# Kernel tuning notes

Hardware: AMD Instinct MI355X
Metric: run time of the kernel (lower is better)

## Reference

```python
import jax, jax.numpy as jnp
import numpy as np

B, D_IN, H1, H2, A = 8192, 512, 4096, 4096, 64
QMIN, QMAX = -128.0, 127.0  # int8 saturation range


def _int_vals(key, shape, spread):
    # integer-valued fixed-point tensor stored as float32
    return jnp.clip(jnp.round(jax.random.normal(key, shape) * spread), QMIN * spread, QMAX * spread).astype(jnp.float32)


def setup_inputs() -> dict:
    key = jax.random.key(0)
    ks = jax.random.split(key, 9)
    x = jnp.clip(jnp.round(jax.random.normal(ks[0], (B, D_IN)) * 32.0), QMIN, QMAX).astype(jnp.float32)
    w1 = jnp.clip(jnp.round(jax.random.normal(ks[1], (H1, D_IN)) * 16.0), QMIN, QMAX).astype(jnp.float32)
    b1 = _int_vals(ks[2], (H1,), 256.0)
    w2 = jnp.clip(jnp.round(jax.random.normal(ks[3], (H2, H1)) * 16.0), QMIN, QMAX).astype(jnp.float32)
    b2 = _int_vals(ks[4], (H2,), 256.0)
    w_mu = jnp.clip(jnp.round(jax.random.normal(ks[5], (A, H2)) * 16.0), QMIN, QMAX).astype(jnp.float32)
    b_mu = _int_vals(ks[6], (A,), 256.0)
    w_prob = jnp.clip(jnp.round(jax.random.normal(ks[7], (A, H2)) * 16.0), QMIN, QMAX).astype(jnp.float32)
    b_prob = _int_vals(ks[8], (A,), 256.0)
    M = jnp.full((1,), 2.0 ** -10, dtype=jnp.float32)  # per-layer requant multiplier
    s = jnp.full((1,), 0.05, dtype=jnp.float32)        # activation quantize scale
    return {
        "x": x, "w1": w1, "b1": b1, "w2": w2, "b2": b2,
        "w_mu": w_mu, "b_mu": b_mu, "w_prob": w_prob, "b_prob": b_prob,
        "M1": M, "M2": M, "M_mu": M, "M_prob": M,
        "s2": s, "s_mu": s, "s_prob": s,
    }


def _qlinear(x, w, b, M):
    # genesys fixed-point linear: int accumulate then requantize by multiplier M
    acc = jnp.matmul(x, w.T) + b  # integer-valued fp32 accumulator
    return jnp.round(M * acc)


def _quantize(src, scale, zero_point=0.0):
    return jnp.clip(jnp.round(src / scale) + zero_point, QMIN, QMAX)


def reference(x, w1, b1, w2, b2, w_mu, b_mu, w_prob, b_prob, M1, M2, M_mu, M_prob, s2, s_mu, s_prob):
    h = jax.nn.relu(_qlinear(x, w1, b1, M1))
    h = _quantize(h, s2)
    h = jax.nn.relu(_qlinear(h, w2, b2, M2))
    # NOTE: original forward_int feeds the un-quantized relu output into the
    # heads (x_mu/x_prob quantizations are dead code) and returns only prob.
    prob = _qlinear(h, w_prob, b_prob, M_prob)
    return prob
```

## Files before the change

kernel.cpp:

```cpp
#include <hip/hip_runtime.h>
#include <stdint.h>

#define NB   8192
#define DIN  512
#define NH1  4096
#define NH2  4096
#define NA   64

typedef int v4i __attribute__((ext_vector_type(4)));

__device__ __forceinline__ v4i mfma_i8(v4i a, v4i b, v4i c) {
    return __builtin_amdgcn_mfma_i32_16x16x64_i8(a, b, c, 0, 0, 0);
}

__device__ __forceinline__ void gload16(const void* g, const void* l) {
    __builtin_amdgcn_global_load_lds(
        (const __attribute__((address_space(1))) void*)(uintptr_t)g,
        (__attribute__((address_space(3))) void*)(uint32_t)(uintptr_t)l,
        16, 0, 0);
}

__global__ void cvt_i8(const float* __restrict__ in, signed char* __restrict__ out, int n4) {
    const int i = blockIdx.x * blockDim.x + threadIdx.x;
    if (i >= n4) return;
    const float4 v = ((const float4*)in)[i];
    char4 c;
    c.x = (signed char)__float2int_rn(v.x);
    c.y = (signed char)__float2int_rn(v.y);
    c.z = (signed char)__float2int_rn(v.z);
    c.w = (signed char)__float2int_rn(v.w);
    ((char4*)out)[i] = c;
}

__global__ void cvt_xfrag(const float* __restrict__ x, signed char* __restrict__ xf) {
    const int u   = blockIdx.x * 256 + threadIdx.x;
    const int g   = u >> 9;
    const int rem = u & 511;
    const int kt  = rem >> 6;
    const int l   = rem & 63;
    const int row = g * 16 + (l & 15);
    const int k0  = kt * 64 + (l >> 4) * 16;
    const float4* src = (const float4*)(x + (size_t)row * DIN + k0);
    signed char v[16];
    #pragma unroll
    for (int q = 0; q < 4; ++q) {
        const float4 f = src[q];
        v[q*4+0] = (signed char)__float2int_rn(f.x);
        v[q*4+1] = (signed char)__float2int_rn(f.y);
        v[q*4+2] = (signed char)__float2int_rn(f.z);
        v[q*4+3] = (signed char)__float2int_rn(f.w);
    }
    *(int4*)(xf + (size_t)u * 16) = *(const int4*)v;
}

__global__ void sum_wp(const float* __restrict__ wp, int* __restrict__ S) {
    __shared__ int red[256];
    const int a = blockIdx.x, t = threadIdx.x;
    int p = 0;
    for (int k = t; k < NH2; k += 256) p += __float2int_rn(wp[(size_t)a * NH2 + k]);
    red[t] = p; __syncthreads();
    for (int s = 128; s > 0; s >>= 1) { if (t < s) red[t] += red[t + s]; __syncthreads(); }
    if (t == 0) S[a] = red[0];
}

template <int EPI>
__global__ __launch_bounds__(512, 4)
void gemm_af(const signed char* __restrict__ Af,
             const signed char* __restrict__ Bg,
             int M, int N, int K,
             const float* __restrict__ bias,
             const float* __restrict__ Mscale,
             const float* __restrict__ qscale,
             signed char* __restrict__ out0,
             signed char* __restrict__ out1)
{
    __shared__ __align__(16) signed char lds[69632];

    const int tid  = threadIdx.x;
    const int lane = tid & 63;
    const int wid  = tid >> 6;
    const int wm   = wid >> 1, wn = wid & 1;

    const int nwg  = gridDim.x;
    const int bid  = blockIdx.x;
    const int swzb = (bid & 7) * (nwg >> 3) + (bid >> 3);
    const int nbx  = N >> 7;
    const int bx   = swzb % nbx;
    const int by   = swzb / nbx;
    const int bm0  = by << 8, bn0 = bx << 7;

    const int srow = tid >> 2;
    const int sc   = (((tid & 3) ^ ((tid >> 3) & 3)) << 4);
    const signed char* bS = Bg + (size_t)(bn0 + srow) * K + sc;

    const int r    = lane & 15;
    const int pc   = (((lane >> 4) ^ ((r >> 1) & 3)) << 4);
    const int boff = wn * 4096 + r * 64 + pc;

    const int NKT = K >> 6;
    const signed char* afB = Af + (((size_t)((bm0 >> 4) + wm * 4) * NKT) << 10) + lane * 16;

    const int nt = K >> 6;

    v4i af[4], bf[4];
    #pragma unroll
    for (int m = 0; m < 4; ++m)
        af[m] = *(const v4i*)(afB + (((size_t)(m * NKT)) << 10));
    gload16(bS,      lds + tid * 16);
    gload16(bS + 64, lds + 8192 + tid * 16);
    asm volatile("s_waitcnt vmcnt(1)" ::: "memory");
    __builtin_amdgcn_s_barrier();

    v4i acc[4][4] = {};

    for (int t = 0; t < nt; ++t) {
        const signed char* L = lds + (t % 3) * 8192;
        #pragma unroll
        for (int n = 0; n < 4; ++n) bf[n] = *(const v4i*)(L + boff + n * 1024);

        const size_t tl = (size_t)((t + 1 < nt) ? (t + 1) : t);

        __builtin_amdgcn_s_setprio(1);
        #pragma unroll
        for (int m = 0; m < 4; ++m) {
            #pragma unroll
            for (int n = 0; n < 4; ++n)
                acc[m][n] = mfma_i8(af[m], bf[n], acc[m][n]);
            af[m] = *(const v4i*)(afB + (((size_t)(m * NKT) + tl) << 10));
        }
        __builtin_amdgcn_s_setprio(0);

        if (t + 2 < nt) {
            gload16(bS + ((t + 2) << 6), lds + ((t + 2) % 3) * 8192 + tid * 16);
            asm volatile("s_waitcnt vmcnt(1)" ::: "memory");
        } else if (t + 1 < nt) {
            asm volatile("s_waitcnt vmcnt(0)" ::: "memory");
        }
        __builtin_amdgcn_s_barrier();
    }

    __syncthreads();
    signed char* img0 = lds;
    signed char* img1 = lds + 34816;
    const int rowb = wm * 64 + ((lane >> 4) << 2);
    const int colb = wn * 64 + (lane & 15);

    if constexpr (EPI == 1) {
        const float Mv = Mscale[0];
        const float sv = qscale[0];
        #pragma unroll
        for (int n = 0; n < 4; ++n) {
            const int col  = colb + n * 16;
            const int bint = __float2int_rn(bias[bn0 + col]);
            #pragma unroll
            for (int m = 0; m < 4; ++m) {
                #pragma unroll
                for (int j = 0; j < 4; ++j) {
                    const int row  = rowb + m * 16 + j;
                    const int accv = acc[m][n][j] + bint;
                    float h = rintf(Mv * (float)accv);
                    h = fmaxf(h, 0.0f);
                    float q = rintf(h / sv);
                    q = fminf(fmaxf(q, -128.0f), 127.0f);
                    img0[row * 136 + col] = (signed char)(int)q;
                }
            }
        }
        __syncthreads();
        const int oNKT = N >> 6;
        #pragma unroll
        for (int i = 0; i < 4; ++i) {
            const int u    = i * 512 + tid;
            const int g_l  = u >> 7;
            const int kt_l = (u >> 6) & 1;
            const int l    = u & 63;
            const int lrow = g_l * 16 + (l & 15);
            const int lcol = kt_l * 64 + (l >> 4) * 16;
            const size_t g  = (size_t)((bm0 >> 4) + g_l);
            const size_t kt = (size_t)((bn0 >> 6) + kt_l);
            *(int4*)(out0 + ((g * oNKT + kt) << 10) + l * 16) =
                *(const int4*)(img0 + lrow * 136 + lcol);
        }
    } else {
        const float Mv = Mscale[0];
        #pragma unroll
        for (int n = 0; n < 4; ++n) {
            const int col  = colb + n * 16;
            const int bint = __float2int_rn(bias[bn0 + col]);
            #pragma unroll
            for (int m = 0; m < 4; ++m) {
                #pragma unroll
                for (int j = 0; j < 4; ++j) {
                    const int row  = rowb + m * 16 + j;
                    const int accv = acc[m][n][j] + bint;
                    double rr = rint((double)Mv * (double)accv);
                    rr = rr > 0.0 ? rr : 0.0;
                    const int v = (int)rr;
                    img0[row * 136 + col] = (signed char)((v & 255) - 128);
                    img1[row * 136 + col] = (signed char)((v >> 8) - 128);
                }
            }
        }
        __syncthreads();
        #pragma unroll
        for (int p = 0; p < 8; ++p) {
            const int idx = p * 512 + tid;
            const int row = idx >> 4;
            const int cb  = (idx & 15) * 8;
            const size_t gaddr = (size_t)(bm0 + row) * N + bn0 + cb;
            *(int2*)(out0 + gaddr) = *(const int2*)(img0 + row * 136 + cb);
            *(int2*)(out1 + gaddr) = *(const int2*)(img1 + row * 136 + cb);
        }
    }
}

__global__ __launch_bounds__(512, 1)
void head_mfma(const signed char* __restrict__ lo,
               const signed char* __restrict__ hi,
               const signed char* __restrict__ wpq,
               int* __restrict__ part)
{
    __shared__ __align__(16) signed char Bl[32768];
    __shared__ __align__(16) signed char Al[3][32768];

    const int tid  = threadIdx.x;
    const int lane = tid & 63;
    const int wid  = tid >> 6;
    const int rblk = blockIdx.x >> 3;
    const int kblk = blockIdx.x & 7;
    const int bm0  = rblk << 8;
    const int kb   = kblk << 9;

    #pragma unroll
    for (int s = 0; s < 4; ++s) {
        const int brow = s * 16 + (tid >> 5);
        const int pch  = tid & 31;
        const int lc   = pch ^ (brow & 7);
        gload16(wpq + (size_t)brow * NH2 + kb + lc * 16, Bl + brow * 512 + pch * 16);
    }

    const int srow  = tid >> 2;
    const int sclog = (tid & 3) ^ ((tid >> 3) & 3);
    const size_t ab = (size_t)(bm0 + srow) * NH2 + kb + sclog * 16;
    const size_t rK = (size_t)128 * NH2;

    #define HSTAGE(bp, ko) do { \
        gload16(lo + ab + (ko),      &Al[bp][0]     + tid * 16); \
        gload16(lo + ab + rK + (ko), &Al[bp][8192]  + tid * 16); \
        gload16(hi + ab + (ko),      &Al[bp][16384] + tid * 16); \
        gload16(hi + ab + rK + (ko), &Al[bp][24576] + tid * 16); } while (0)

    HSTAGE(0, 0);
    HSTAGE(1, 64);

    const int r    = lane & 15;
    const int cg   = lane >> 4;
    const int pcA  = (cg ^ ((r >> 1) & 3)) * 16;
    const int aoff = wid * 2048 + r * 64 + pcA;

    v4i accL[2][4] = {}, accH[2][4] = {};
    int cur = 0, nxt = 2;

    for (int t = 0; t < 8; ++t) {
        if (t < 7) asm volatile("s_waitcnt vmcnt(4)" ::: "memory");
        else       asm volatile("s_waitcnt vmcnt(0)" ::: "memory");
        __builtin_amdgcn_s_barrier();

        const signed char* A = &Al[cur][0];
        v4i bf[4], al[2], ah[2];
        #pragma unroll
        for (int n = 0; n < 4; ++n)
            bf[n] = *(const v4i*)(Bl + (n * 16 + r) * 512 + (((t * 4 + cg) ^ (r & 7)) * 16));
        #pragma unroll
        for (int m = 0; m < 2; ++m) al[m] = *(const v4i*)(A + aoff + m * 1024);
        #pragma unroll
        for (int m = 0; m < 2; ++m) ah[m] = *(const v4i*)(A + 16384 + aoff + m * 1024);

        if (t + 2 < 8) HSTAGE(nxt, (t + 2) << 6);

        __builtin_amdgcn_s_setprio(1);
        #pragma unroll
        for (int m = 0; m < 2; ++m)
            #pragma unroll
            for (int n = 0; n < 4; ++n) {
                accL[m][n] = mfma_i8(al[m], bf[n], accL[m][n]);
                accH[m][n] = mfma_i8(ah[m], bf[n], accH[m][n]);
            }
        __builtin_amdgcn_s_setprio(0);
        __builtin_amdgcn_s_barrier();

        cur = (cur == 2) ? 0 : cur + 1;
        nxt = (nxt == 2) ? 0 : nxt + 1;
    }
    #undef HSTAGE

    int* pb = part + (size_t)kblk * (NB * NA);
    const int rowb = bm0 + wid * 32 + ((lane >> 4) << 2);
    #pragma unroll
    for (int m = 0; m < 2; ++m)
        #pragma unroll
        for (int n = 0; n < 4; ++n) {
            const int a = n * 16 + (lane & 15);
            #pragma unroll
            for (int j = 0; j < 4; ++j) {
                const int row = rowb + m * 16 + j;
                pb[(size_t)row * NA + a] = accL[m][n][j] + (accH[m][n][j] << 8);
            }
        }
}

__global__ __launch_bounds__(256)
void comb_head(const int* __restrict__ part, const int* __restrict__ S,
               const float* __restrict__ bp, const float* __restrict__ Mp,
               float* __restrict__ out)
{
    const int t = blockIdx.x * 256 + threadIdx.x;
    const int a = t & 63;
    long long sum = 0;
    #pragma unroll
    for (int c = 0; c < 8; ++c) sum += part[(size_t)c * (NB * NA) + t];
    sum += 32896LL * (long long)S[a] + (long long)__float2int_rn(bp[a]);
    out[t] = (float)rint((double)Mp[0] * (double)sum);
}

extern "C" void kernel_launch(void* const* d_in, const int* in_sizes, int n_in,
                              void* d_out, int out_size, void* d_ws, size_t ws_size,
                              hipStream_t stream) {
    const float* x  = (const float*)d_in[0];
    const float* w1 = (const float*)d_in[1];
    const float* b1 = (const float*)d_in[2];
    const float* w2 = (const float*)d_in[3];
    const float* b2 = (const float*)d_in[4];
    const float* wp = (const float*)d_in[7];
    const float* bp = (const float*)d_in[8];
    const float* M1 = (const float*)d_in[9];
    const float* M2 = (const float*)d_in[10];
    const float* Mp = (const float*)d_in[12];
    const float* s2 = (const float*)d_in[13];

    const size_t MB = (size_t)1 << 20;
    char* ws = (char*)d_ws;
    signed char* xf    = (signed char*)(ws);
    signed char* w1_i8 = (signed char*)(ws + 4  * MB);
    signed char* w2_i8 = (signed char*)(ws + 6  * MB);
    signed char* wp_i8 = (signed char*)(ws + 22 * MB);
    int*         Ssum  = (int*)        (ws + 22 * MB + 512 * 1024);
    signed char* h1f   = (signed char*)(ws + 23 * MB);
    signed char* h2lo  = (signed char*)(ws + 55 * MB);
    signed char* h2hi  = (signed char*)(ws + 87 * MB);
    int*         part  = (int*)        (ws);

    cvt_xfrag<<<dim3(1024), dim3(256), 0, stream>>>(x, xf);
    cvt_i8<<<dim3(2048),  dim3(256), 0, stream>>>(w1, w1_i8, NH1 * DIN / 4);
    cvt_i8<<<dim3(16384), dim3(256), 0, stream>>>(w2, w2_i8, NH2 * NH1 / 4);
    cvt_i8<<<dim3(256),   dim3(256), 0, stream>>>(wp, wp_i8, NA  * NH2 / 4);
    sum_wp<<<dim3(64), dim3(256), 0, stream>>>(wp, Ssum);

    gemm_af<1><<<dim3((NB / 256) * (NH1 / 128)), dim3(512), 0, stream>>>(
        xf, w1_i8, NB, NH1, DIN, b1, M1, s2, h1f, nullptr);
    gemm_af<2><<<dim3((NB / 256) * (NH2 / 128)), dim3(512), 0, stream>>>(
        h1f, w2_i8, NB, NH2, NH1, b2, M2, nullptr, h2lo, h2hi);
    head_mfma<<<dim3(256), dim3(512), 0, stream>>>(h2lo, h2hi, wp_i8, part);
    comb_head<<<dim3(NB * NA / 256), dim3(256), 0, stream>>>(part, Ssum, bp, Mp, (float*)d_out);
}
```

Before: 208.8 us.

## Fuse prob head into layer-2 GEMM epilogue with atomic accumulation; merge prep kernels

Removes the separate head_mfma kernel. Each layer-2 GEMM tile now multiplies its lo/hi split int8 activations, held in LDS, by the matching K-slice of the fragment-ordered head weights, then atomically adds 64-bit partial sums into a zeroed buffer. This avoids writing the two 32 MB h2 planes to global memory and reading them back. The four conversion kernels and the weight-sum kernel are merged into one launch, and the LDS row stride changes from 136 to 144. The cost is heavy 64-bit global atomic traffic, since each output element gets one add per N-tile (32 per element), plus an extra memset.

```diff
diff --git a/kernel.cpp b/kernel.cpp
--- a/kernel.cpp
+++ b/kernel.cpp
@@ -20,47 +20,72 @@
         16, 0, 0);
 }
 
-__global__ void cvt_i8(const float* __restrict__ in, signed char* __restrict__ out, int n4) {
-    const int i = blockIdx.x * blockDim.x + threadIdx.x;
-    if (i >= n4) return;
-    const float4 v = ((const float4*)in)[i];
-    char4 c;
-    c.x = (signed char)__float2int_rn(v.x);
-    c.y = (signed char)__float2int_rn(v.y);
-    c.z = (signed char)__float2int_rn(v.z);
-    c.w = (signed char)__float2int_rn(v.w);
-    ((char4*)out)[i] = c;
-}
-
-__global__ void cvt_xfrag(const float* __restrict__ x, signed char* __restrict__ xf) {
-    const int u   = blockIdx.x * 256 + threadIdx.x;
-    const int g   = u >> 9;
-    const int rem = u & 511;
-    const int kt  = rem >> 6;
-    const int l   = rem & 63;
-    const int row = g * 16 + (l & 15);
-    const int k0  = kt * 64 + (l >> 4) * 16;
-    const float4* src = (const float4*)(x + (size_t)row * DIN + k0);
-    signed char v[16];
-    #pragma unroll
-    for (int q = 0; q < 4; ++q) {
-        const float4 f = src[q];
-        v[q*4+0] = (signed char)__float2int_rn(f.x);
-        v[q*4+1] = (signed char)__float2int_rn(f.y);
-        v[q*4+2] = (signed char)__float2int_rn(f.z);
-        v[q*4+3] = (signed char)__float2int_rn(f.w);
+__global__ __launch_bounds__(256)
+void prep(const float* __restrict__ x,  const float* __restrict__ w1,
+          const float* __restrict__ w2, const float* __restrict__ wp,
+          signed char* __restrict__ xf, signed char* __restrict__ w1_i8,
+          signed char* __restrict__ w2_i8, signed char* __restrict__ wpf,
+          int* __restrict__ S)
+{
+    __shared__ int red[256];
+    const int b   = blockIdx.x;
+    const int tid = threadIdx.x;
+
+    if (b < 18432) {
+        const float* in  = (b < 16384) ? w2 : w1;
+        signed char* out = (b < 16384) ? w2_i8 : w1_i8;
+        const int i = ((b < 16384) ? b : (b - 16384)) * 256 + tid;
+        const float4 v = ((const float4*)in)[i];
+        char4 c;
+        c.x = (signed char)__float2int_rn(v.x);
+        c.y = (signed char)__float2int_rn(v.y);
+        c.z = (signed char)__float2int_rn(v.z);
+        c.w = (signed char)__float2int_rn(v.w);
+        ((char4*)out)[i] = c;
+    } else if (b < 19456) {
+        const int u   = (b - 18432) * 256 + tid;
+        const int g   = u >> 9;
+        const int kt  = (u >> 6) & 7;
+        const int l   = u & 63;
+        const int row = g * 16 + (l & 15);
+        const int k0  = kt * 64 + (l >> 4) * 16;
+        const float4* src = (const float4*)(x + (size_t)row * DIN + k0);
+        signed char v[16];
+        #pragma unroll
+        for (int q = 0; q < 4; ++q) {
+            const float4 f = src[q];
+            v[q*4+0] = (signed char)__float2int_rn(f.x);
+            v[q*4+1] = (signed char)__float2int_rn(f.y);
+            v[q*4+2] = (signed char)__float2int_rn(f.z);
+            v[q*4+3] = (signed char)__float2int_rn(f.w);
+        }
+        *(int4*)(xf + (size_t)u * 16) = *(const int4*)v;
+    } else if (b < 19520) {
+        const int u   = (b - 19456) * 256 + tid;
+        const int g   = u >> 12;
+        const int kt  = (u >> 6) & 63;
+        const int l   = u & 63;
+        const int row = g * 16 + (l & 15);
+        const int k0  = kt * 64 + (l >> 4) * 16;
+        const float4* src = (const float4*)(wp + (size_t)row * NH2 + k0);
+        signed char v[16];
+        #pragma unroll
+        for (int q = 0; q < 4; ++q) {
+            const float4 f = src[q];
+            v[q*4+0] = (signed char)__float2int_rn(f.x);
+            v[q*4+1] = (signed char)__float2int_rn(f.y);
+            v[q*4+2] = (signed char)__float2int_rn(f.z);
+            v[q*4+3] = (signed char)__float2int_rn(f.w);
+        }
+        *(int4*)(wpf + (size_t)u * 16) = *(const int4*)v;
+    } else {
+        const int a = b - 19520;
+        int p = 0;
+        for (int k = tid; k < NH2; k += 256) p += __float2int_rn(wp[(size_t)a * NH2 + k]);
+        red[tid] = p; __syncthreads();
+        for (int s = 128; s > 0; s >>= 1) { if (tid < s) red[tid] += red[tid + s]; __syncthreads(); }
+        if (tid == 0) S[a] = red[0];
     }
-    *(int4*)(xf + (size_t)u * 16) = *(const int4*)v;
-}
-
-__global__ void sum_wp(const float* __restrict__ wp, int* __restrict__ S) {
-    __shared__ int red[256];
-    const int a = blockIdx.x, t = threadIdx.x;
-    int p = 0;
-    for (int k = t; k < NH2; k += 256) p += __float2int_rn(wp[(size_t)a * NH2 + k]);
-    red[t] = p; __syncthreads();
-    for (int s = 128; s > 0; s >>= 1) { if (t < s) red[t] += red[t + s]; __syncthreads(); }
-    if (t == 0) S[a] = red[0];
 }
 
 template <int EPI>
@@ -72,9 +97,10 @@
              const float* __restrict__ Mscale,
              const float* __restrict__ qscale,
              signed char* __restrict__ out0,
-             signed char* __restrict__ out1)
+             const signed char* __restrict__ wpf,
+             unsigned long long* __restrict__ part)
 {
-    __shared__ __align__(16) signed char lds[69632];
+    __shared__ __align__(16) signed char lds[73728];
 
     const int tid  = threadIdx.x;
     const int lane = tid & 63;
@@ -141,7 +167,7 @@
 
     __syncthreads();
     signed char* img0 = lds;
-    signed char* img1 = lds + 34816;
+    signed char* img1 = lds + 36864;
     const int rowb = wm * 64 + ((lane >> 4) << 2);
     const int colb = wn * 64 + (lane & 15);
 
@@ -162,7 +188,7 @@
                     h = fmaxf(h, 0.0f);
                     float q = rintf(h / sv);
                     q = fminf(fmaxf(q, -128.0f), 127.0f);
-                    img0[row * 136 + col] = (signed char)(int)q;
+                    img0[row * 144 + col] = (signed char)(int)q;
                 }
             }
         }
@@ -179,7 +205,7 @@
             const size_t g  = (size_t)((bm0 >> 4) + g_l);
             const size_t kt = (size_t)((bn0 >> 6) + kt_l);
             *(int4*)(out0 + ((g * oNKT + kt) << 10) + l * 16) =
-                *(const int4*)(img0 + lrow * 136 + lcol);
+                *(const int4*)(img0 + lrow * 144 + lcol);
         }
     } else {
         const float Mv = Mscale[0];
@@ -196,129 +222,60 @@
                     double rr = rint((double)Mv * (double)accv);
                     rr = rr > 0.0 ? rr : 0.0;
                     const int v = (int)rr;
-                    img0[row * 136 + col] = (signed char)((v & 255) - 128);
-                    img1[row * 136 + col] = (signed char)((v >> 8) - 128);
+                    img0[row * 144 + col] = (signed char)((v & 255) - 128);
+                    img1[row * 144 + col] = (signed char)((v >> 8) - 128);
                 }
             }
         }
         __syncthreads();
-        #pragma unroll
-        for (int p = 0; p < 8; ++p) {
-            const int idx = p * 512 + tid;
-            const int row = idx >> 4;
-            const int cb  = (idx & 15) * 8;
-            const size_t gaddr = (size_t)(bm0 + row) * N + bn0 + cb;
-            *(int2*)(out0 + gaddr) = *(const int2*)(img0 + row * 136 + cb);
-            *(int2*)(out1 + gaddr) = *(const int2*)(img1 + row * 136 + cb);
+
+        v4i bh[4][2];
+        #pragma unroll
+        for (int n = 0; n < 4; ++n)
+            #pragma unroll
+            for (int kk = 0; kk < 2; ++kk)
+                bh[n][kk] = *(const v4i*)(wpf + (((size_t)(n * 64 + (bn0 >> 6) + kk)) << 10) + lane * 16);
+
+        v4i accL[2][4] = {}, accH[2][4] = {};
+        #pragma unroll
+        for (int mm = 0; mm < 2; ++mm) {
+            const int arow = (wid * 2 + mm) * 16 + (lane & 15);
+            #pragma unroll
+            for (int kk = 0; kk < 2; ++kk) {
+                const int ka = kk * 64 + (lane >> 4) * 16;
+                const v4i aL = *(const v4i*)(img0 + arow * 144 + ka);
+                const v4i aH = *(const v4i*)(img1 + arow * 144 + ka);
+                #pragma unroll
+                for (int n = 0; n < 4; ++n) {
+                    accL[mm][n] = mfma_i8(aL, bh[n][kk], accL[mm][n]);
+                    accH[mm][n] = mfma_i8(aH, bh[n][kk], accH[mm][n]);
+                }
+            }
+        }
+        #pragma unroll
+        for (int mm = 0; mm < 2; ++mm) {
+            #pragma unroll
+            for (int n = 0; n < 4; ++n) {
+                const int a = n * 16 + (lane & 15);
+                #pragma unroll
+                for (int j = 0; j < 4; ++j) {
+                    const int row = bm0 + (wid * 2 + mm) * 16 + ((lane >> 4) << 2) + j;
+                    const long long val = (long long)accL[mm][n][j] + 256LL * (long long)accH[mm][n][j];
+                    atomicAdd(part + (size_t)row * NA + a, (unsigned long long)val);
+                }
+            }
         }
     }
 }
 
-__global__ __launch_bounds__(512, 1)
-void head_mfma(const signed char* __restrict__ lo,
-               const signed char* __restrict__ hi,
-               const signed char* __restrict__ wpq,
-               int* __restrict__ part)
-{
-    __shared__ __align__(16) signed char Bl[32768];
-    __shared__ __align__(16) signed char Al[3][32768];
-
-    const int tid  = threadIdx.x;
-    const int lane = tid & 63;
-    const int wid  = tid >> 6;
-    const int rblk = blockIdx.x >> 3;
-    const int kblk = blockIdx.x & 7;
-    const int bm0  = rblk << 8;
-    const int kb   = kblk << 9;
-
-    #pragma unroll
-    for (int s = 0; s < 4; ++s) {
-        const int brow = s * 16 + (tid >> 5);
-        const int pch  = tid & 31;
-        const int lc   = pch ^ (brow & 7);
-        gload16(wpq + (size_t)brow * NH2 + kb + lc * 16, Bl + brow * 512 + pch * 16);
-    }
-
-    const int srow  = tid >> 2;
-    const int sclog = (tid & 3) ^ ((tid >> 3) & 3);
-    const size_t ab = (size_t)(bm0 + srow) * NH2 + kb + sclog * 16;
-    const size_t rK = (size_t)128 * NH2;
-
-    #define HSTAGE(bp, ko) do { \
-        gload16(lo + ab + (ko),      &Al[bp][0]     + tid * 16); \
-        gload16(lo + ab + rK + (ko), &Al[bp][8192]  + tid * 16); \
-        gload16(hi + ab + (ko),      &Al[bp][16384] + tid * 16); \
-        gload16(hi + ab + rK + (ko), &Al[bp][24576] + tid * 16); } while (0)
-
-    HSTAGE(0, 0);
-    HSTAGE(1, 64);
-
-    const int r    = lane & 15;
-    const int cg   = lane >> 4;
-    const int pcA  = (cg ^ ((r >> 1) & 3)) * 16;
-    const int aoff = wid * 2048 + r * 64 + pcA;
-
-    v4i accL[2][4] = {}, accH[2][4] = {};
-    int cur = 0, nxt = 2;
-
-    for (int t = 0; t < 8; ++t) {
-        if (t < 7) asm volatile("s_waitcnt vmcnt(4)" ::: "memory");
-        else       asm volatile("s_waitcnt vmcnt(0)" ::: "memory");
-        __builtin_amdgcn_s_barrier();
-
-        const signed char* A = &Al[cur][0];
-        v4i bf[4], al[2], ah[2];
-        #pragma unroll
-        for (int n = 0; n < 4; ++n)
-            bf[n] = *(const v4i*)(Bl + (n * 16 + r) * 512 + (((t * 4 + cg) ^ (r & 7)) * 16));
-        #pragma unroll
-        for (int m = 0; m < 2; ++m) al[m] = *(const v4i*)(A + aoff + m * 1024);
-        #pragma unroll
-        for (int m = 0; m < 2; ++m) ah[m] = *(const v4i*)(A + 16384 + aoff + m * 1024);
-
-        if (t + 2 < 8) HSTAGE(nxt, (t + 2) << 6);
-
-        __builtin_amdgcn_s_setprio(1);
-        #pragma unroll
-        for (int m = 0; m < 2; ++m)
-            #pragma unroll
-            for (int n = 0; n < 4; ++n) {
-                accL[m][n] = mfma_i8(al[m], bf[n], accL[m][n]);
-                accH[m][n] = mfma_i8(ah[m], bf[n], accH[m][n]);
-            }
-        __builtin_amdgcn_s_setprio(0);
-        __builtin_amdgcn_s_barrier();
-
-        cur = (cur == 2) ? 0 : cur + 1;
-        nxt = (nxt == 2) ? 0 : nxt + 1;
-    }
-    #undef HSTAGE
-
-    int* pb = part + (size_t)kblk * (NB * NA);
-    const int rowb = bm0 + wid * 32 + ((lane >> 4) << 2);
-    #pragma unroll
-    for (int m = 0; m < 2; ++m)
-        #pragma unroll
-        for (int n = 0; n < 4; ++n) {
-            const int a = n * 16 + (lane & 15);
-            #pragma unroll
-            for (int j = 0; j < 4; ++j) {
-                const int row = rowb + m * 16 + j;
-                pb[(size_t)row * NA + a] = accL[m][n][j] + (accH[m][n][j] << 8);
-            }
-        }
-}
-
 __global__ __launch_bounds__(256)
-void comb_head(const int* __restrict__ part, const int* __restrict__ S,
+void comb_head(const unsigned long long* __restrict__ part, const int* __restrict__ S,
                const float* __restrict__ bp, const float* __restrict__ Mp,
                float* __restrict__ out)
 {
     const int t = blockIdx.x * 256 + threadIdx.x;
     const int a = t & 63;
-    long long sum = 0;
-    #pragma unroll
-    for (int c = 0; c < 8; ++c) sum += part[(size_t)c * (NB * NA) + t];
+    long long sum = (long long)part[t];
     sum += 32896LL * (long long)S[a] + (long long)__float2int_rn(bp[a]);
     out[t] = (float)rint((double)Mp[0] * (double)sum);
 }
@@ -343,23 +300,20 @@
     signed char* xf    = (signed char*)(ws);
     signed char* w1_i8 = (signed char*)(ws + 4  * MB);
     signed char* w2_i8 = (signed char*)(ws + 6  * MB);
-    signed char* wp_i8 = (signed char*)(ws + 22 * MB);
+    signed char* wpf   = (signed char*)(ws + 22 * MB);
     int*         Ssum  = (int*)        (ws + 22 * MB + 512 * 1024);
     signed char* h1f   = (signed char*)(ws + 23 * MB);
-    signed char* h2lo  = (signed char*)(ws + 55 * MB);
-    signed char* h2hi  = (signed char*)(ws + 87 * MB);
-    int*         part  = (int*)        (ws);
-
-    cvt_xfrag<<<dim3(1024), dim3(256), 0, stream>>>(x, xf);
-    cvt_i8<<<dim3(2048),  dim3(256), 0, stream>>>(w1, w1_i8, NH1 * DIN / 4);
-    cvt_i8<<<dim3(16384), dim3(256), 0, stream>>>(w2, w2_i8, NH2 * NH1 / 4);
-    cvt_i8<<<dim3(256),   dim3(256), 0, stream>>>(wp, wp_i8, NA  * NH2 / 4);
-    sum_wp<<<dim3(64), dim3(256), 0, stream>>>(wp, Ssum);
+    unsigned long long* part = (unsigned long long*)(ws + 55 * MB);
+
+    prep<<<dim3(19584), dim3(256), 0, stream>>>(x, w1, w2, wp, xf, w1_i8, w2_i8, wpf, Ssum);
 
     gemm_af<1><<<dim3((NB / 256) * (NH1 / 128)), dim3(512), 0, stream>>>(
-        xf, w1_i8, NB, NH1, DIN, b1, M1, s2, h1f, nullptr);
+        xf, w1_i8, NB, NH1, DIN, b1, M1, s2, h1f, nullptr, nullptr);
+
+    hipMemsetAsync(part, 0, (size_t)NB * NA * 8, stream);
+
     gemm_af<2><<<dim3((NB / 256) * (NH2 / 128)), dim3(512), 0, stream>>>(
-        h1f, w2_i8, NB, NH2, NH1, b2, M2, nullptr, h2lo, h2hi);
-    head_mfma<<<dim3(256), dim3(512), 0, stream>>>(h2lo, h2hi, wp_i8, part);
+        h1f, w2_i8, NB, NH2, NH1, b2, M2, nullptr, nullptr, wpf, part);
+
     comb_head<<<dim3(NB * NA / 256), dim3(256), 0, stream>>>(part, Ssum, bp, Mp, (float*)d_out);
 }
```

Measured after the change: 257.8 us. +23.4%, slower.
